# Kernel tuning notes

Measured on AMD Instinct MI355X. Metric: run time of the kernel, lower is better.

## Reference

```python
import jax, jax.numpy as jnp
import numpy as np

B, C, H, W = 2, 256, 32, 32
PK, CK = 256, 256


def setup_inputs() -> dict:
    key = jax.random.key(0)
    ks = jax.random.split(key, 9)
    s = 1.0 / np.sqrt(C)
    return {
        'x': jax.random.normal(ks[0], (B, C, H, W), jnp.float32),
        'primary_indices': jax.random.randint(ks[1], (B, PK), 0, B * H * W),
        'compare_indices': jax.random.randint(ks[2], (B, CK), 0, B * H * W),
        'pre_w': jax.random.uniform(ks[3], (3, C, C), jnp.float32, -s, s),
        'pre_b': jax.random.uniform(ks[4], (3, C), jnp.float32, -s, s),
        'post_w': jax.random.uniform(ks[5], (2, C, C), jnp.float32, -s, s),
        'post_b': jax.random.uniform(ks[6], (2, C), jnp.float32, -s, s),
        'post_out_w': jax.random.uniform(ks[7], (2, C), jnp.float32, -s, s),
        'post_out_b': jax.random.uniform(ks[8], (2,), jnp.float32, -s, s),
    }


def reference(x, primary_indices, compare_indices, pre_w, pre_b,
              post_w, post_b, post_out_w, post_out_b):
    # pre_compare: stack of 1x1 convs (c->c->c->c), ReLU between layers
    h = x
    for i in range(3):
        h = jnp.einsum('bchw,oc->bohw', h, pre_w[i]) + pre_b[i][None, :, None, None]
        if i < 2:
            h = jax.nn.relu(h)
    bs, c, hh, ww = h.shape
    # flatten to [bs*h*w, c] node features (matches torch transpose+reshape)
    flat = h.reshape(bs, c, hh * ww).transpose(0, 2, 1).reshape(bs * hh * ww, c)
    # gather primary / compare node features with global flat indices
    xp = flat[primary_indices.reshape(-1)].reshape(bs, -1, c).transpose(0, 2, 1)  # [b,c,pk]
    xc = flat[compare_indices.reshape(-1)].reshape(bs, -1, c).transpose(0, 2, 1)  # [b,c,ck]
    # broadcast pairwise squared difference -> [b,c,pk,ck]
    xx = (xp[:, :, :, None] - xc[:, :, None, :]) ** 2
    # post_compare: 1x1 conv stack c->c->c->2, ReLU between layers
    g = xx
    for i in range(2):
        g = jax.nn.relu(jnp.einsum('bcpq,oc->bopq', g, post_w[i]) + post_b[i][None, :, None, None])
    out = jnp.einsum('bcpq,oc->bopq', g, post_out_w) + post_out_b[None, :, None, None]
    return out  # [b, 2, pk, ck]
```

## Files before the change

kernel.cpp:

```cpp
#include <hip/hip_runtime.h>

typedef unsigned short u16;
typedef short bf16x8 __attribute__((ext_vector_type(8)));
typedef float f32x4 __attribute__((ext_vector_type(4)));
typedef u16 u16x4 __attribute__((ext_vector_type(4)));

__device__ __forceinline__ float b2f(u16 h) {
  unsigned u = ((unsigned)h) << 16;
  return __builtin_bit_cast(float, u);
}
__device__ __forceinline__ u16 f2b(float f) {
  unsigned u = __builtin_bit_cast(unsigned, f);
  u = u + 0x7fffu + ((u >> 16) & 1u);
  return (u16)(u >> 16);
}
__device__ __forceinline__ void gld_lds16(const void* g, void* l) {
  __builtin_amdgcn_global_load_lds(
      (__attribute__((address_space(1))) void*)(g),
      (__attribute__((address_space(3))) void*)(l), 16, 0, 0);
}

__global__ void dense_edge_prep(const float* __restrict__ x,
                                const float* __restrict__ pre_w,
                                const float* __restrict__ post_w,
                                u16* __restrict__ wb, u16* __restrict__ xt) {
  const int blk = blockIdx.x;
  const int t = threadIdx.x;
  if (blk < 160) {
    const int id = blk * 256 + t;
    const int layer = id >> 13;
    const int sid = id & 8191;
    const int m = sid >> 5;
    const int s8 = sid & 31;
    const float* src = (layer < 2) ? (post_w + layer * 65536)
                                   : (pre_w + (layer - 2) * 65536);
    u16* dst = wb + layer * 65536;
    f32x4 a = *(const f32x4*)(src + m * 256 + s8 * 8);
    f32x4 c = *(const f32x4*)(src + m * 256 + s8 * 8 + 4);
    bf16x8 o;
#pragma unroll
    for (int j = 0; j < 4; j++) o[j] = (short)f2b(a[j]);
#pragma unroll
    for (int j = 0; j < 4; j++) o[4 + j] = (short)f2b(c[j]);
    *(bf16x8*)(dst + (s8 * 256 + m) * 8) = o;
  } else {
    __shared__ float tile[32 * 65];
    const int xb = blk - 160;
    const int b = xb >> 7;
    const int ct = (xb >> 4) & 7;
    const int ht = xb & 15;
    const int c0 = ct * 32, hw0 = ht * 64;
#pragma unroll
    for (int rep = 0; rep < 8; rep++) {
      const int idx = rep * 256 + t;
      const int cl = idx >> 6, hl = idx & 63;
      tile[cl * 65 + hl] = x[(b * 256 + c0 + cl) * 1024 + hw0 + hl];
    }
    __syncthreads();
    const int hl = t >> 2, c8 = t & 3;
    bf16x8 o;
#pragma unroll
    for (int i = 0; i < 8; i++) o[i] = (short)f2b(tile[(c8 * 8 + i) * 65 + hl]);
    *(bf16x8*)(xt + (b * 1024 + hw0 + hl) * 256 + c0 + c8 * 8) = o;
  }
}

__global__ __launch_bounds__(256, 2) void dense_edge_pre(
    const u16* __restrict__ xt, const u16* __restrict__ wpre,
    const float* __restrict__ preb, u16* __restrict__ flat) {
  __shared__ u16 feat[2][4096];
  const int t = threadIdx.x;
  const int wv = t >> 6, ln = t & 63;
  const int nb = blockIdx.x * 16;
  const int q4 = ln >> 4, r15 = ln & 15;

#pragma unroll
  for (int i = 0; i < 2; i++) {
    const int slot = wv * 128 + i * 64 + ln;
    const int s8 = slot >> 4, nl = slot & 15;
    gld_lds16(xt + (nb + nl) * 256 + s8 * 8, &feat[0][slot * 8]);
  }
  __syncthreads();

#pragma unroll
  for (int l = 0; l < 3; l++) {
    const u16* wl = wpre + l * 65536;
    f32x4 acc[4];
    f32x4 zero = {0.f, 0.f, 0.f, 0.f};
#pragma unroll
    for (int mt = 0; mt < 4; mt++) acc[mt] = zero;
#pragma unroll
    for (int s = 0; s < 8; s++) {
      bf16x8 bv = *(const bf16x8*)(&feat[l & 1][((s * 4 + q4) * 16 + r15) * 8]);
#pragma unroll
      for (int mt = 0; mt < 4; mt++) {
        bf16x8 av = *(const bf16x8*)(wl + ((s * 4 + q4) * 256 + wv * 64 + mt * 16 + r15) * 8);
        acc[mt] = __builtin_amdgcn_mfma_f32_16x16x32_bf16(av, bv, acc[mt], 0, 0, 0);
      }
    }
    if (l < 2) {
#pragma unroll
      for (int mt = 0; mt < 4; mt++) {
        const int o = wv * 64 + mt * 16 + q4 * 4;
        f32x4 bb = *(const f32x4*)(preb + l * 256 + o);
        u16x4 pk;
#pragma unroll
        for (int r = 0; r < 4; r++) {
          float v = fmaxf(acc[mt][r] + bb[r], 0.f);
          pk[r] = f2b(v);
        }
        *(u16x4*)(&feat[(l + 1) & 1][((o >> 3) * 16 + r15) * 8 + (o & 7)]) = pk;
      }
      __syncthreads();
    } else {
#pragma unroll
      for (int mt = 0; mt < 4; mt++) {
        const int o = wv * 64 + mt * 16 + q4 * 4;
        f32x4 bb = *(const f32x4*)(preb + 512 + o);
        u16x4 pk;
#pragma unroll
        for (int r = 0; r < 4; r++) pk[r] = f2b(acc[mt][r] + bb[r]);
        *(u16x4*)(flat + (nb + r15) * 256 + o) = pk;
      }
    }
  }
}

__global__ __launch_bounds__(512, 2) void dense_edge_main(
    const u16* __restrict__ flat, const int* __restrict__ pidx,
    const int* __restrict__ cidx, const u16* __restrict__ w1s,
    const u16* __restrict__ w2s, const float* __restrict__ b1,
    const float* __restrict__ b2, const float* __restrict__ w3,
    const float* __restrict__ b3, float* __restrict__ out) {
  __shared__ u16 xxbuf[16384];
  __shared__ u16 t1buf[16384];
  __shared__ float pbuf[4][2][64];

  const int t = threadIdx.x;
  const int wv = t >> 6;
  const int ln = t & 63;
  const int q4 = ln >> 4, r15 = ln & 15;
  const bool prod = wv < 4;
  const int cw = wv & 3;
  const int blk = blockIdx.x;
  const int tile0 = blk * 8;
  const int b = tile0 >> 10;
  const int pt = (tile0 >> 5) & 31;
  const int qt0 = tile0 & 31;
  const int p0 = pt * 8;

  const u16* wsrc = prod ? w1s : w2s;
  bf16x8 af_w[4][8];
#pragma unroll
  for (int s = 0; s < 8; s++)
#pragma unroll
    for (int mt = 0; mt < 4; mt++)
      af_w[mt][s] = *(const bf16x8*)(wsrc + ((s * 4 + q4) * 256 + cw * 64 + mt * 16 + r15) * 8);

  int pn = 0;
  if (prod) pn = pidx[b * 256 + p0 + (ln >> 3)];
  const u16* prow = flat + pn * 256 + cw * 64;

#pragma unroll 1
  for (int j = 0; j <= 8; j++) {
    if (prod) {
      if (j < 8) {
        const int qn = cidx[b * 256 + (qt0 + j) * 8 + (ln & 7)];
        const u16* qrow = flat + qn * 256 + cw * 64;
#pragma unroll
        for (int i = 0; i < 8; i++) {
          bf16x8 av = *(const bf16x8*)(prow + i * 8);
          bf16x8 bv = *(const bf16x8*)(qrow + i * 8);
          bf16x8 ov;
#pragma unroll
          for (int jj = 0; jj < 8; jj++) {
            float d = b2f((u16)av[jj]) - b2f((u16)bv[jj]);
            ov[jj] = (short)f2b(d * d);
          }
          *(bf16x8*)(xxbuf + ((cw * 8 + i) * 64 + ln) * 8) = ov;
        }
      }
    } else if (j > 0) {
      f32x4 acc[4][4];
      {
        f32x4 zero = {0.f, 0.f, 0.f, 0.f};
#pragma unroll
        for (int mt = 0; mt < 4; mt++)
#pragma unroll
          for (int nt = 0; nt < 4; nt++) acc[mt][nt] = zero;
      }
#pragma unroll
      for (int s = 0; s < 8; s++) {
        bf16x8 bfr[4];
#pragma unroll
        for (int nt = 0; nt < 4; nt++)
          bfr[nt] = *(const bf16x8*)(t1buf + ((s * 4 + q4) * 64 + nt * 16 + r15) * 8);
#pragma unroll
        for (int mt = 0; mt < 4; mt++)
#pragma unroll
          for (int nt = 0; nt < 4; nt++)
            acc[mt][nt] = __builtin_amdgcn_mfma_f32_16x16x32_bf16(af_w[mt][s], bfr[nt], acc[mt][nt], 0, 0, 0);
      }
      float part[2][4] = {{0.f, 0.f, 0.f, 0.f}, {0.f, 0.f, 0.f, 0.f}};
#pragma unroll
      for (int mt = 0; mt < 4; mt++) {
        const int o = cw * 64 + mt * 16 + q4 * 4;
        f32x4 bb = *(const f32x4*)(b2 + o);
        f32x4 w3a = *(const f32x4*)(w3 + o);
        f32x4 w3b = *(const f32x4*)(w3 + 256 + o);
#pragma unroll
        for (int nt = 0; nt < 4; nt++) {
#pragma unroll
          for (int r = 0; r < 4; r++) {
            float v = fmaxf(acc[mt][nt][r] + bb[r], 0.f);
            part[0][nt] += v * w3a[r];
            part[1][nt] += v * w3b[r];
          }
        }
      }
#pragma unroll
      for (int o3 = 0; o3 < 2; o3++)
#pragma unroll
        for (int nt = 0; nt < 4; nt++) {
          part[o3][nt] += __shfl_xor(part[o3][nt], 16, 64);
          part[o3][nt] += __shfl_xor(part[o3][nt], 32, 64);
        }
      if (q4 == 0) {
#pragma unroll
        for (int o3 = 0; o3 < 2; o3++)
#pragma unroll
          for (int nt = 0; nt < 4; nt++)
            pbuf[cw][o3][nt * 16 + r15] = part[o3][nt];
      }
    }
    __syncthreads();

    if (prod) {
      if (j < 8) {
        f32x4 acc[4][4];
        {
          f32x4 zero = {0.f, 0.f, 0.f, 0.f};
#pragma unroll
          for (int mt = 0; mt < 4; mt++)
#pragma unroll
            for (int nt = 0; nt < 4; nt++) acc[mt][nt] = zero;
        }
#pragma unroll
        for (int s = 0; s < 8; s++) {
          bf16x8 bfr[4];
#pragma unroll
          for (int nt = 0; nt < 4; nt++)
            bfr[nt] = *(const bf16x8*)(xxbuf + ((s * 4 + q4) * 64 + nt * 16 + r15) * 8);
#pragma unroll
          for (int mt = 0; mt < 4; mt++)
#pragma unroll
            for (int nt = 0; nt < 4; nt++)
              acc[mt][nt] = __builtin_amdgcn_mfma_f32_16x16x32_bf16(af_w[mt][s], bfr[nt], acc[mt][nt], 0, 0, 0);
        }
#pragma unroll
        for (int mt = 0; mt < 4; mt++) {
          const int o = cw * 64 + mt * 16 + q4 * 4;
          f32x4 bb = *(const f32x4*)(b1 + o);
#pragma unroll
          for (int nt = 0; nt < 4; nt++) {
            const int nn = nt * 16 + r15;
            u16x4 pk;
#pragma unroll
            for (int r = 0; r < 4; r++) {
              float v = fmaxf(acc[mt][nt][r] + bb[r], 0.f);
              pk[r] = f2b(v);
            }
            *(u16x4*)(t1buf + ((o >> 3) * 64 + nn) * 8 + (o & 7)) = pk;
          }
        }
      }
    } else if (j > 0) {
      const int idx = t & 255;
      if (idx < 128) {
        const int o3 = idx >> 6;
        const int n = idx & 63;
        float v = pbuf[0][o3][n] + pbuf[1][o3][n] + pbuf[2][o3][n] + pbuf[3][o3][n] + b3[o3];
        out[((b * 2 + o3) * 256 + p0 + (n >> 3)) * 256 + (qt0 + j - 1) * 8 + (n & 7)] = v;
      }
    }
    __syncthreads();
  }
}

extern "C" void kernel_launch(void* const* d_in, const int* in_sizes, int n_in,
                              void* d_out, int out_size, void* d_ws, size_t ws_size,
                              hipStream_t stream) {
  (void)in_sizes; (void)n_in; (void)out_size; (void)ws_size;
  const float* x          = (const float*)d_in[0];
  const int*   pidx       = (const int*)d_in[1];
  const int*   cidx       = (const int*)d_in[2];
  const float* pre_w      = (const float*)d_in[3];
  const float* pre_b      = (const float*)d_in[4];
  const float* post_w     = (const float*)d_in[5];
  const float* post_b     = (const float*)d_in[6];
  const float* post_out_w = (const float*)d_in[7];
  const float* post_out_b = (const float*)d_in[8];
  float* out = (float*)d_out;

  u16* ws   = (u16*)d_ws;
  u16* wb   = ws;
  u16* w1s  = wb;
  u16* w2s  = wb + 65536;
  u16* wpre = wb + 131072;
  u16* xt   = ws + 327680;
  u16* flat = ws + 851968;

  dense_edge_prep<<<416, 256, 0, stream>>>(x, pre_w, post_w, wb, xt);
  dense_edge_pre<<<128, 256, 0, stream>>>(xt, wpre, pre_b, flat);
  dense_edge_main<<<256, 512, 0, stream>>>(flat, pidx, cidx, w1s, w2s,
                                           post_b, post_b + 256,
                                           post_out_w, post_out_b, out);
}
```

Before: 122.9 us.

## Software-pipeline edge main kernel with double-buffered LDS and staged gathers

Restructures the main kernel into a software pipeline. Producer waves compute layer-1 GEMM for tile j while building the squared-difference tile for j+1, and consumer waves run layer-2 for tile j-1, with one barrier per step instead of two. Tiles shrink to 8x4 pairs (16 per block), LDS buffers are double-buffered, and primary/compare rows are staged into LDS via global_load_lds instead of per-lane global reads. It also uses the native bf16 conversion and raises MFMA priority, at the cost of more LDS, smaller MFMA N tiles and more loop iterations.

```diff
diff --git a/kernel.cpp b/kernel.cpp
--- a/kernel.cpp
+++ b/kernel.cpp
@@ -10,9 +10,7 @@
   return __builtin_bit_cast(float, u);
 }
 __device__ __forceinline__ u16 f2b(float f) {
-  unsigned u = __builtin_bit_cast(unsigned, f);
-  u = u + 0x7fffu + ((u >> 16) & 1u);
-  return (u16)(u >> 16);
+  return __builtin_bit_cast(u16, (__bf16)f);
 }
 __device__ __forceinline__ void gld_lds16(const void* g, void* l) {
   __builtin_amdgcn_global_load_lds(
@@ -126,15 +124,18 @@
   }
 }
 
+#define NTILE 16
 __global__ __launch_bounds__(512, 2) void dense_edge_main(
     const u16* __restrict__ flat, const int* __restrict__ pidx,
     const int* __restrict__ cidx, const u16* __restrict__ w1s,
     const u16* __restrict__ w2s, const float* __restrict__ b1,
     const float* __restrict__ b2, const float* __restrict__ w3,
     const float* __restrict__ b3, float* __restrict__ out) {
-  __shared__ u16 xxbuf[16384];
-  __shared__ u16 t1buf[16384];
-  __shared__ float pbuf[4][2][64];
+  __shared__ u16 xxbuf[2][8192];
+  __shared__ u16 t1buf[2][8192];
+  __shared__ u16 pstage[2048];
+  __shared__ u16 qstage[2][1024];
+  __shared__ float pbuf[2][4][2][32];
 
   const int t = threadIdx.x;
   const int wv = t >> 6;
@@ -143,148 +144,195 @@
   const bool prod = wv < 4;
   const int cw = wv & 3;
   const int blk = blockIdx.x;
-  const int tile0 = blk * 8;
-  const int b = tile0 >> 10;
-  const int pt = (tile0 >> 5) & 31;
-  const int qt0 = tile0 & 31;
+  const int b = blk >> 7;
+  const int pt = (blk >> 2) & 31;
+  const int qg = blk & 3;
   const int p0 = pt * 8;
+  const int q0 = qg * 64;
 
   const u16* wsrc = prod ? w1s : w2s;
-  bf16x8 af_w[4][8];
+  bf16x8 af[4][8];
 #pragma unroll
   for (int s = 0; s < 8; s++)
 #pragma unroll
     for (int mt = 0; mt < 4; mt++)
-      af_w[mt][s] = *(const bf16x8*)(wsrc + ((s * 4 + q4) * 256 + cw * 64 + mt * 16 + r15) * 8);
-
-  int pn = 0;
-  if (prod) pn = pidx[b * 256 + p0 + (ln >> 3)];
-  const u16* prow = flat + pn * 256 + cw * 64;
+      af[mt][s] = *(const bf16x8*)(wsrc + ((s * 4 + q4) * 256 + cw * 64 + mt * 16 + r15) * 8);
+
+  if (prod) {
+    const int slot = cw * 64 + ln;
+    const int prow = slot & 7, cc = slot >> 3;
+    const int pn = pidx[b * 256 + p0 + prow];
+    gld_lds16(flat + pn * 256 + cc * 8, &pstage[slot * 8]);
+  } else {
+    const int half = (wv - 4) >> 1;
+    const int slot = ((wv - 4) & 1) * 64 + ln;
+    const int cc = slot >> 2, qrow = slot & 3;
+    const int qn = cidx[b * 256 + q0 + half * 4 + qrow];
+    gld_lds16(flat + qn * 256 + cc * 8, &qstage[half][slot * 8]);
+  }
+  const int gslot = (wv >= 6) ? (wv - 6) * 64 + ln : 0;
+  int qn_cur = 0;
+  if (wv >= 6) qn_cur = cidx[b * 256 + q0 + 8 + (gslot & 3)];
+  __syncthreads();
+
+  const int nn32 = ln & 31;
+  const int half32 = ln >> 5;
+  bf16x8 pa[4];
+  if (prod) {
+#pragma unroll
+    for (int i = 0; i < 4; i++) {
+      const int cc = cw * 8 + half32 * 4 + i;
+      pa[i] = *(const bf16x8*)(&pstage[((cc * 8 + (nn32 >> 2))) * 8]);
+    }
+  }
+
+  auto do_xx = [&](int jx) {
+    const u16* qs = qstage[jx & 1];
+    u16* xb = xxbuf[jx & 1];
+#pragma unroll
+    for (int i = 0; i < 4; i++) {
+      const int cc = cw * 8 + half32 * 4 + i;
+      bf16x8 av = pa[i];
+      bf16x8 bv = *(const bf16x8*)(&qs[(cc * 4 + (nn32 & 3)) * 8]);
+      bf16x8 ov;
+#pragma unroll
+      for (int jj = 0; jj < 8; jj++) {
+        float d = b2f((u16)av[jj]) - b2f((u16)bv[jj]);
+        ov[jj] = (short)f2b(d * d);
+      }
+      *(bf16x8*)(&xb[(cc * 32 + nn32) * 8]) = ov;
+    }
+  };
+
+  auto do_g1 = [&](int jg) {
+    const u16* xb = xxbuf[jg & 1];
+    f32x4 acc[4][2];
+    {
+      f32x4 zero = {0.f, 0.f, 0.f, 0.f};
+#pragma unroll
+      for (int mt = 0; mt < 4; mt++)
+#pragma unroll
+        for (int nt = 0; nt < 2; nt++) acc[mt][nt] = zero;
+    }
+    __builtin_amdgcn_s_setprio(1);
+#pragma unroll
+    for (int s = 0; s < 8; s++) {
+      bf16x8 bfr[2];
+#pragma unroll
+      for (int nt = 0; nt < 2; nt++)
+        bfr[nt] = *(const bf16x8*)(xb + ((s * 4 + q4) * 32 + nt * 16 + r15) * 8);
+#pragma unroll
+      for (int mt = 0; mt < 4; mt++)
+#pragma unroll
+        for (int nt = 0; nt < 2; nt++)
+          acc[mt][nt] = __builtin_amdgcn_mfma_f32_16x16x32_bf16(af[mt][s], bfr[nt], acc[mt][nt], 0, 0, 0);
+    }
+    __builtin_amdgcn_s_setprio(0);
+#pragma unroll
+    for (int mt = 0; mt < 4; mt++) {
+      const int o = cw * 64 + mt * 16 + q4 * 4;
+      f32x4 bb = *(const f32x4*)(b1 + o);
+#pragma unroll
+      for (int nt = 0; nt < 2; nt++) {
+        const int n = nt * 16 + r15;
+        u16x4 pk;
+#pragma unroll
+        for (int r = 0; r < 4; r++) {
+          float v = fmaxf(acc[mt][nt][r] + bb[r], 0.f);
+          pk[r] = f2b(v);
+        }
+        *(u16x4*)(&t1buf[jg & 1][((o >> 3) * 32 + n) * 8 + (o & 7)]) = pk;
+      }
+    }
+  };
+
+  auto do_g2 = [&](int jg) {
+    const u16* tb = t1buf[jg & 1];
+    f32x4 acc[4][2];
+    {
+      f32x4 zero = {0.f, 0.f, 0.f, 0.f};
+#pragma unroll
+      for (int mt = 0; mt < 4; mt++)
+#pragma unroll
+        for (int nt = 0; nt < 2; nt++) acc[mt][nt] = zero;
+    }
+    __builtin_amdgcn_s_setprio(1);
+#pragma unroll
+    for (int s = 0; s < 8; s++) {
+      bf16x8 bfr[2];
+#pragma unroll
+      for (int nt = 0; nt < 2; nt++)
+        bfr[nt] = *(const bf16x8*)(tb + ((s * 4 + q4) * 32 + nt * 16 + r15) * 8);
+#pragma unroll
+      for (int mt = 0; mt < 4; mt++)
+#pragma unroll
+        for (int nt = 0; nt < 2; nt++)
+          acc[mt][nt] = __builtin_amdgcn_mfma_f32_16x16x32_bf16(af[mt][s], bfr[nt], acc[mt][nt], 0, 0, 0);
+    }
+    __builtin_amdgcn_s_setprio(0);
+    float part[2][2] = {{0.f, 0.f}, {0.f, 0.f}};
+#pragma unroll
+    for (int mt = 0; mt < 4; mt++) {
+      const int o = cw * 64 + mt * 16 + q4 * 4;
+      f32x4 bb = *(const f32x4*)(b2 + o);
+      f32x4 w3a = *(const f32x4*)(w3 + o);
+      f32x4 w3b = *(const f32x4*)(w3 + 256 + o);
+#pragma unroll
+      for (int nt = 0; nt < 2; nt++) {
+#pragma unroll
+        for (int r = 0; r < 4; r++) {
+          float v = fmaxf(acc[mt][nt][r] + bb[r], 0.f);
+          part[0][nt] += v * w3a[r];
+          part[1][nt] += v * w3b[r];
+        }
+      }
+    }
+#pragma unroll
+    for (int o3 = 0; o3 < 2; o3++)
+#pragma unroll
+      for (int nt = 0; nt < 2; nt++) {
+        part[o3][nt] += __shfl_xor(part[o3][nt], 16, 64);
+        part[o3][nt] += __shfl_xor(part[o3][nt], 32, 64);
+      }
+    if (q4 == 0) {
+#pragma unroll
+      for (int o3 = 0; o3 < 2; o3++)
+#pragma unroll
+        for (int nt = 0; nt < 2; nt++)
+          pbuf[jg & 1][cw][o3][nt * 16 + r15] = part[o3][nt];
+    }
+  };
+
+  auto do_out = [&](int jo) {
+    const int o3 = ln >> 5, n = ln & 31;
+    float v = b3[o3];
+#pragma unroll
+    for (int k = 0; k < 4; k++) v += pbuf[jo & 1][k][o3][n];
+    out[((b * 2 + o3) * 256 + p0 + (n >> 2)) * 256 + q0 + jo * 4 + (n & 3)] = v;
+  };
+
+  if (prod) do_xx(0);
+  __syncthreads();
 
 #pragma unroll 1
-  for (int j = 0; j <= 8; j++) {
+  for (int j = 0; j <= NTILE; j++) {
     if (prod) {
-      if (j < 8) {
-        const int qn = cidx[b * 256 + (qt0 + j) * 8 + (ln & 7)];
-        const u16* qrow = flat + qn * 256 + cw * 64;
-#pragma unroll
-        for (int i = 0; i < 8; i++) {
-          bf16x8 av = *(const bf16x8*)(prow + i * 8);
-          bf16x8 bv = *(const bf16x8*)(qrow + i * 8);
-          bf16x8 ov;
-#pragma unroll
-          for (int jj = 0; jj < 8; jj++) {
-            float d = b2f((u16)av[jj]) - b2f((u16)bv[jj]);
-            ov[jj] = (short)f2b(d * d);
-          }
-          *(bf16x8*)(xxbuf + ((cw * 8 + i) * 64 + ln) * 8) = ov;
-        }
-      }
-    } else if (j > 0) {
-      f32x4 acc[4][4];
-      {
-        f32x4 zero = {0.f, 0.f, 0.f, 0.f};
-#pragma unroll
-        for (int mt = 0; mt < 4; mt++)
-#pragma unroll
-          for (int nt = 0; nt < 4; nt++) acc[mt][nt] = zero;
-      }
-#pragma unroll
-      for (int s = 0; s < 8; s++) {
-        bf16x8 bfr[4];
-#pragma unroll
-        for (int nt = 0; nt < 4; nt++)
-          bfr[nt] = *(const bf16x8*)(t1buf + ((s * 4 + q4) * 64 + nt * 16 + r15) * 8);
-#pragma unroll
-        for (int mt = 0; mt < 4; mt++)
-#pragma unroll
-          for (int nt = 0; nt < 4; nt++)
-            acc[mt][nt] = __builtin_amdgcn_mfma_f32_16x16x32_bf16(af_w[mt][s], bfr[nt], acc[mt][nt], 0, 0, 0);
-      }
-      float part[2][4] = {{0.f, 0.f, 0.f, 0.f}, {0.f, 0.f, 0.f, 0.f}};
-#pragma unroll
-      for (int mt = 0; mt < 4; mt++) {
-        const int o = cw * 64 + mt * 16 + q4 * 4;
-        f32x4 bb = *(const f32x4*)(b2 + o);
-        f32x4 w3a = *(const f32x4*)(w3 + o);
-        f32x4 w3b = *(const f32x4*)(w3 + 256 + o);
-#pragma unroll
-        for (int nt = 0; nt < 4; nt++) {
-#pragma unroll
-          for (int r = 0; r < 4; r++) {
-            float v = fmaxf(acc[mt][nt][r] + bb[r], 0.f);
-            part[0][nt] += v * w3a[r];
-            part[1][nt] += v * w3b[r];
-          }
-        }
-      }
-#pragma unroll
-      for (int o3 = 0; o3 < 2; o3++)
-#pragma unroll
-        for (int nt = 0; nt < 4; nt++) {
-          part[o3][nt] += __shfl_xor(part[o3][nt], 16, 64);
-          part[o3][nt] += __shfl_xor(part[o3][nt], 32, 64);
-        }
-      if (q4 == 0) {
-#pragma unroll
-        for (int o3 = 0; o3 < 2; o3++)
-#pragma unroll
-          for (int nt = 0; nt < 4; nt++)
-            pbuf[cw][o3][nt * 16 + r15] = part[o3][nt];
-      }
+      if (j < NTILE) do_g1(j);
+      if (j < NTILE - 1) do_xx(j + 1);
+    } else {
+      if (wv == 4 && j >= 2) do_out(j - 2);
+      if (wv >= 6 && j < NTILE - 2) {
+        gld_lds16(flat + qn_cur * 256 + (gslot >> 2) * 8,
+                  &qstage[j & 1][gslot * 8]);
+        if (j < NTILE - 3)
+          qn_cur = cidx[b * 256 + q0 + (j + 3) * 4 + (gslot & 3)];
+      }
+      if (j >= 1) do_g2(j - 1);
     }
     __syncthreads();
-
-    if (prod) {
-      if (j < 8) {
-        f32x4 acc[4][4];
-        {
-          f32x4 zero = {0.f, 0.f, 0.f, 0.f};
-#pragma unroll
-          for (int mt = 0; mt < 4; mt++)
-#pragma unroll
-            for (int nt = 0; nt < 4; nt++) acc[mt][nt] = zero;
-        }
-#pragma unroll
-        for (int s = 0; s < 8; s++) {
-          bf16x8 bfr[4];
-#pragma unroll
-          for (int nt = 0; nt < 4; nt++)
-            bfr[nt] = *(const bf16x8*)(xxbuf + ((s * 4 + q4) * 64 + nt * 16 + r15) * 8);
-#pragma unroll
-          for (int mt = 0; mt < 4; mt++)
-#pragma unroll
-            for (int nt = 0; nt < 4; nt++)
-              acc[mt][nt] = __builtin_amdgcn_mfma_f32_16x16x32_bf16(af_w[mt][s], bfr[nt], acc[mt][nt], 0, 0, 0);
-        }
-#pragma unroll
-        for (int mt = 0; mt < 4; mt++) {
-          const int o = cw * 64 + mt * 16 + q4 * 4;
-          f32x4 bb = *(const f32x4*)(b1 + o);
-#pragma unroll
-          for (int nt = 0; nt < 4; nt++) {
-            const int nn = nt * 16 + r15;
-            u16x4 pk;
-#pragma unroll
-            for (int r = 0; r < 4; r++) {
-              float v = fmaxf(acc[mt][nt][r] + bb[r], 0.f);
-              pk[r] = f2b(v);
-            }
-            *(u16x4*)(t1buf + ((o >> 3) * 64 + nn) * 8 + (o & 7)) = pk;
-          }
-        }
-      }
-    } else if (j > 0) {
-      const int idx = t & 255;
-      if (idx < 128) {
-        const int o3 = idx >> 6;
-        const int n = idx & 63;
-        float v = pbuf[0][o3][n] + pbuf[1][o3][n] + pbuf[2][o3][n] + pbuf[3][o3][n] + b3[o3];
-        out[((b * 2 + o3) * 256 + p0 + (n >> 3)) * 256 + (qt0 + j - 1) * 8 + (n & 7)] = v;
-      }
-    }
-    __syncthreads();
-  }
+  }
+
+  if (wv == 4) do_out(NTILE - 1);
 }
 
 extern "C" void kernel_launch(void* const* d_in, const int* in_sizes, int n_in,
```

Measured after the change: 117.7 us. -4.3%, faster.
